# Kernel optimization log

Measured on AMD Instinct MI355X. Metric: run time of the kernel, lower is better.

Reference implementation:

```python
import jax, jax.numpy as jnp
import numpy as np

B, T, C, K, NH, HID, L, NC = 16, 500, 512, 7, 8, 2048, 3, 2
HD = C // NH
SCALE = float(1.0 / np.sqrt(HD))


def setup_inputs() -> dict:
    key = jax.random.key(0)
    ks = jax.random.split(key, 24)
    rn = lambda k, sh, s=0.02: jax.random.normal(k, sh, jnp.float32) * s
    return {
        'x': jax.random.normal(ks[0], (B, T, C), jnp.float32),
        'dw_w': rn(ks[1], (L, NC, C, 1, K)),   # depthwise conv kernels (groups=C)
        'dw_b': rn(ks[2], (L, NC, C)),
        'pw_w': rn(ks[3], (L, NC, C, C)),       # pointwise 1x1 conv weights [out,in]
        'pw_b': rn(ks[4], (L, NC, C)),
        'cln_g': jnp.ones((L, NC, C), jnp.float32),
        'cln_b': jnp.zeros((L, NC, C), jnp.float32),
        'wq': rn(ks[5], (L, C, C)), 'bq': rn(ks[6], (L, C)),
        'wk': rn(ks[7], (L, C, C)), 'bk': rn(ks[8], (L, C)),
        'wv': rn(ks[9], (L, C, C)), 'bv': rn(ks[10], (L, C)),
        'wo': rn(ks[11], (L, C, C)), 'bo': rn(ks[12], (L, C)),
        'aln_g': jnp.ones((L, C), jnp.float32), 'aln_b': jnp.zeros((L, C), jnp.float32),
        'w1': rn(ks[13], (L, HID, C)), 'b1': rn(ks[14], (L, HID)),
        'w2': rn(ks[15], (L, C, HID)), 'b2': rn(ks[16], (L, C)),
        'fln_g': jnp.ones((L, C), jnp.float32), 'fln_b': jnp.zeros((L, C), jnp.float32),
    }


def _ln(x, g, b):
    m = x.mean(-1, keepdims=True)
    v = ((x - m) ** 2).mean(-1, keepdims=True)
    return (x - m) / jnp.sqrt(v + 1e-5) * g + b


def _conv_block(x, w, b, pw, pb, g, be):
    # x: (B, C, T). Depthwise conv (groups=C), padding K//2 keeps T.
    out = jax.lax.conv_general_dilated(
        x, w, window_strides=(1,), padding=[(K // 2, K // 2)],
        feature_group_count=C, dimension_numbers=('NCH', 'OIH', 'NCH')) + b[None, :, None]
    out = jnp.einsum('bct,oc->bot', out, pw) + pb[None, :, None]  # pointwise 1x1
    out = _ln(out.transpose(0, 2, 1), g, be).transpose(0, 2, 1)
    return out


def _attn(x, wq, bq, wk, bk, wv, bv, wo, bo):
    Bx, Tx, Cx = x.shape
    def split(h):
        return h.reshape(Bx, Tx, NH, HD).transpose(0, 2, 1, 3)  # (B,H,T,HD)
    q = split(x @ wq.T + bq)
    k = split(x @ wk.T + bk)
    v = split(x @ wv.T + bv)
    att = jnp.einsum('bhqd,bhkd->bhqk', q, k) * SCALE
    mask = jnp.tril(jnp.ones((Tx, Tx), bool))
    att = jnp.where(mask, att, -1e10)
    att = jax.nn.softmax(att, axis=-1)
    y = jnp.einsum('bhqk,bhkd->bhqd', att, v)
    y = y.transpose(0, 2, 1, 3).reshape(Bx, Tx, Cx)
    return y @ wo.T + bo


def _block(x, l, dw_w, dw_b, pw_w, pw_b, cln_g, cln_b, wq, bq, wk, bk, wv, bv,
           wo, bo, aln_g, aln_b, w1, b1, w2, b2, fln_g, fln_b):
    out = x.transpose(0, 2, 1)  # (B, C, T)
    for c in range(NC):
        out = _conv_block(out, dw_w[l, c], dw_b[l, c], pw_w[l, c], pw_b[l, c],
                          cln_g[l, c], cln_b[l, c])
    out = out.transpose(0, 2, 1)  # (B, T, C)
    out = _attn(out, wq[l], bq[l], wk[l], bk[l], wv[l], bv[l], wo[l], bo[l])
    out = _ln(out, aln_g[l], aln_b[l])
    out = _ln(jax.nn.relu(out @ w1[l].T + b1[l]) @ w2[l].T + b2[l], fln_g[l], fln_b[l])
    return out  # eval mode: dropouts are identity


def reference(x, dw_w, dw_b, pw_w, pw_b, cln_g, cln_b, wq, bq, wk, bk, wv, bv,
              wo, bo, aln_g, aln_b, w1, b1, w2, b2, fln_g, fln_b):
    outs = []
    h = x
    for l in range(L):
        h = _block(h, l, dw_w, dw_b, pw_w, pw_b, cln_g, cln_b, wq, bq, wk, bk,
                   wv, bv, wo, bo, aln_g, aln_b, w1, b1, w2, b2, fln_g, fln_b)
        outs.append(h)
    return tuple(outs)
```

## Files before the change

### kernel.cpp

```cpp
#include <hip/hip_runtime.h>
#include <hip/hip_bf16.h>

namespace {
constexpr int B = 16, T = 500, C = 512, KW = 7, NH = 8, HD = 64, HID = 2048;
constexpr int M = B * T;
constexpr float SCALE = 0.125f;
constexpr int BTC = B * T * C;
constexpr int CC = C * C;
constexpr int SEG_PW0 = 0;
constexpr int SEG_PW1 = CC;
constexpr int SEG_WQ  = 2 * CC;
constexpr int SEG_WK  = 3 * CC;
constexpr int SEG_WV  = 4 * CC;
constexpr int SEG_WO  = 5 * CC;
constexpr int SEG_W1  = 6 * CC;
constexpr int SEG_W2  = 6 * CC + HID * C;
constexpr int SEG_END = 6 * CC + 2 * HID * C;
}

typedef short s16x8 __attribute__((ext_vector_type(8)));
typedef float f32x4v __attribute__((ext_vector_type(4)));
typedef unsigned short u16x4 __attribute__((ext_vector_type(4)));

__device__ __forceinline__ unsigned int bfrne(float f) {
  unsigned int u = __float_as_uint(f);
  return (u + 0x7fffu + ((u >> 16) & 1u)) >> 16;
}
__device__ __forceinline__ unsigned int pack2(float a, float b) {
  return bfrne(a) | (bfrne(b) << 16);
}

__global__ __launch_bounds__(256) void cvtw_kernel(
    const float* __restrict__ pw0, const float* __restrict__ pw1,
    const float* __restrict__ wqp, const float* __restrict__ wkp,
    const float* __restrict__ wvp, const float* __restrict__ wop,
    const float* __restrict__ w1p, const float* __restrict__ w2p,
    unsigned short* __restrict__ dst) {
  size_t e = ((size_t)blockIdx.x * 256 + threadIdx.x) * 8;
  const float* src;
  size_t off;
  if      (e < SEG_PW1) { src = pw0; off = e - SEG_PW0; }
  else if (e < SEG_WQ)  { src = pw1; off = e - SEG_PW1; }
  else if (e < SEG_WK)  { src = wqp; off = e - SEG_WQ; }
  else if (e < SEG_WV)  { src = wkp; off = e - SEG_WK; }
  else if (e < SEG_WO)  { src = wvp; off = e - SEG_WV; }
  else if (e < SEG_W1)  { src = wop; off = e - SEG_WO; }
  else if (e < SEG_W2)  { src = w1p; off = e - SEG_W1; }
  else                  { src = w2p; off = e - SEG_W2; }
  float4 a = *(const float4*)(src + off);
  float4 b = *(const float4*)(src + off + 4);
  uint4 o;
  o.x = pack2(a.x, a.y); o.y = pack2(a.z, a.w);
  o.z = pack2(b.x, b.y); o.w = pack2(b.z, b.w);
  *(uint4*)(dst + e) = o;
}

__global__ __launch_bounds__(256) void biascat_kernel(
    const float* __restrict__ bq, const float* __restrict__ bk,
    const float* __restrict__ bv, float* __restrict__ dst) {
  int i = blockIdx.x * 256 + threadIdx.x;
  float v = (i < 512) ? bq[i] : (i < 1024 ? bk[i - 512] : bv[i - 1024]);
  dst[i] = v;
}

template <bool XBF, bool RELU, bool YBF>
__global__ __launch_bounds__(256) void gemm_mfma(
    const void* __restrict__ Xv, const unsigned short* __restrict__ Wb,
    const float* __restrict__ bias, void* __restrict__ Yv, int N, int K) {
  __shared__ unsigned short As[2][128 * 40];
  __shared__ unsigned short Bs[2][128 * 40];
  const int tid = threadIdx.x;
  const int n0 = blockIdx.x * 128, m0 = blockIdx.y * 128;
  const int w = tid >> 6, lane = tid & 63;
  const int mh = (w & 1) * 64, nh = (w >> 1) * 64;
  const int quad = lane >> 4, r15 = lane & 15;

  const int row0 = tid >> 2,           kq0 = (tid & 3) * 8;
  const int row1 = (tid + 256) >> 2,   kq1 = (tid & 3) * 8;
  const int xr0 = min(m0 + row0, M - 1), xr1 = min(m0 + row1, M - 1);
  const int wr0 = n0 + row0, wr1 = n0 + row1;

  f32x4v acc[4][4];
#pragma unroll
  for (int i = 0; i < 4; ++i)
#pragma unroll
    for (int j = 0; j < 4; ++j) acc[i][j] = {0.f, 0.f, 0.f, 0.f};

  auto loadX = [&](int k0, int xr, int kq) -> uint4 {
    if (XBF) {
      return *(const uint4*)((const unsigned short*)Xv + (size_t)xr * K + k0 + kq);
    } else {
      const float* xp = (const float*)Xv + (size_t)xr * K + k0 + kq;
      float4 a = *(const float4*)xp;
      float4 b = *(const float4*)(xp + 4);
      uint4 o;
      o.x = pack2(a.x, a.y); o.y = pack2(a.z, a.w);
      o.z = pack2(b.x, b.y); o.w = pack2(b.z, b.w);
      return o;
    }
  };
  auto loadW = [&](int k0, int wr, int kq) -> uint4 {
    return *(const uint4*)(Wb + (size_t)wr * K + k0 + kq);
  };

  uint4 xv0 = loadX(0, xr0, kq0), xv1 = loadX(0, xr1, kq1);
  uint4 wv0 = loadW(0, wr0, kq0), wv1 = loadW(0, wr1, kq1);
  *(uint4*)&As[0][row0 * 40 + kq0] = xv0;
  *(uint4*)&As[0][row1 * 40 + kq1] = xv1;
  *(uint4*)&Bs[0][row0 * 40 + kq0] = wv0;
  *(uint4*)&Bs[0][row1 * 40 + kq1] = wv1;
  int cur = 0;
  const int nk = K / 32;
  for (int c = 0; c < nk; ++c) {
    __syncthreads();
    if (c + 1 < nk) {
      int k0 = (c + 1) * 32;
      xv0 = loadX(k0, xr0, kq0); xv1 = loadX(k0, xr1, kq1);
      wv0 = loadW(k0, wr0, kq0); wv1 = loadW(k0, wr1, kq1);
    }
    const unsigned short* Ac = As[cur];
    const unsigned short* Bc = Bs[cur];
    s16x8 af[4], bg[4];
#pragma unroll
    for (int im = 0; im < 4; ++im)
      af[im] = *(const s16x8*)&Ac[(mh + im * 16 + r15) * 40 + quad * 8];
#pragma unroll
    for (int in = 0; in < 4; ++in)
      bg[in] = *(const s16x8*)&Bc[(nh + in * 16 + r15) * 40 + quad * 8];
#pragma unroll
    for (int in = 0; in < 4; ++in)
#pragma unroll
      for (int im = 0; im < 4; ++im)
        acc[im][in] = __builtin_amdgcn_mfma_f32_16x16x32_bf16(
            af[im], bg[in], acc[im][in], 0, 0, 0);
    if (c + 1 < nk) {
      int nx = cur ^ 1;
      *(uint4*)&As[nx][row0 * 40 + kq0] = xv0;
      *(uint4*)&As[nx][row1 * 40 + kq1] = xv1;
      *(uint4*)&Bs[nx][row0 * 40 + kq0] = wv0;
      *(uint4*)&Bs[nx][row1 * 40 + kq1] = wv1;
      cur = nx;
    }
  }
#pragma unroll
  for (int in = 0; in < 4; ++in) {
    int col = n0 + nh + in * 16 + r15;
    float bv = bias[col];
#pragma unroll
    for (int im = 0; im < 4; ++im) {
      int rowb = m0 + mh + im * 16 + quad * 4;
#pragma unroll
      for (int r = 0; r < 4; ++r) {
        int row = rowb + r;
        if (row < M) {
          float v = acc[im][in][r] + bv;
          if (RELU) v = fmaxf(v, 0.f);
          if (YBF)
            ((unsigned short*)Yv)[(size_t)row * N + col] =
                (unsigned short)bfrne(v);
          else
            ((float*)Yv)[(size_t)row * N + col] = v;
        }
      }
    }
  }
}

__global__ __launch_bounds__(256) void dwconv_kernel(
    const float* __restrict__ X, const float* __restrict__ W,
    const float* __restrict__ bias, unsigned short* __restrict__ Y) {
  int gid = blockIdx.x * 256 + threadIdx.x;
  int b = blockIdx.y;
  int e = gid * 2;
  int t = e >> 9;
  int c = e & 511;
  float acc0 = bias[c], acc1 = bias[c + 1];
  size_t base = (size_t)b * T * C;
#pragma unroll
  for (int k = 0; k < KW; ++k) {
    int tt = t + k - 3;
    if (tt >= 0 && tt < T) {
      float2 xv = *(const float2*)&X[base + (size_t)tt * C + c];
      acc0 += xv.x * W[c * KW + k];
      acc1 += xv.y * W[(c + 1) * KW + k];
    }
  }
  *(unsigned int*)&Y[base + e] = pack2(acc0, acc1);
}

template <bool DUAL>
__global__ __launch_bounds__(256) void ln_kernel(
    const float* __restrict__ X, const float* __restrict__ g,
    const float* __restrict__ bta, float* __restrict__ Y,
    unsigned short* __restrict__ Yb) {
  int row = blockIdx.x * 4 + (threadIdx.x >> 6);
  int lane = threadIdx.x & 63;
  const float* x = X + (size_t)row * C + lane * 8;
  float4 a = *(const float4*)x;
  float4 b2 = *(const float4*)(x + 4);
  float v[8] = {a.x, a.y, a.z, a.w, b2.x, b2.y, b2.z, b2.w};
  float s = 0.f, ss = 0.f;
#pragma unroll
  for (int i = 0; i < 8; ++i) {
    s += v[i];
    ss += v[i] * v[i];
  }
#pragma unroll
  for (int off = 32; off; off >>= 1) {
    s += __shfl_xor(s, off);
    ss += __shfl_xor(ss, off);
  }
  float mean = s * (1.f / C);
  float var = ss * (1.f / C) - mean * mean;
  var = fmaxf(var, 0.f);
  float rstd = rsqrtf(var + 1e-5f);
  float4 g0 = *(const float4*)(g + lane * 8);
  float4 g1 = *(const float4*)(g + lane * 8 + 4);
  float4 be0 = *(const float4*)(bta + lane * 8);
  float4 be1 = *(const float4*)(bta + lane * 8 + 4);
  float gg[8] = {g0.x, g0.y, g0.z, g0.w, g1.x, g1.y, g1.z, g1.w};
  float bb[8] = {be0.x, be0.y, be0.z, be0.w, be1.x, be1.y, be1.z, be1.w};
  float o[8];
#pragma unroll
  for (int i = 0; i < 8; ++i) o[i] = (v[i] - mean) * rstd * gg[i] + bb[i];
  float* y = Y + (size_t)row * C + lane * 8;
  float4 w0 = {o[0], o[1], o[2], o[3]};
  float4 w1 = {o[4], o[5], o[6], o[7]};
  *(float4*)y = w0;
  *(float4*)(y + 4) = w1;
  if (DUAL) {
    uint4 ob;
    ob.x = pack2(o[0], o[1]); ob.y = pack2(o[2], o[3]);
    ob.z = pack2(o[4], o[5]); ob.w = pack2(o[6], o[7]);
    *(uint4*)(Yb + (size_t)row * C + lane * 8) = ob;
  }
}

__global__ __launch_bounds__(256) void attn_mfma_kernel(
    const unsigned short* __restrict__ QKV, unsigned short* __restrict__ Yb) {
  constexpr int QS = 3 * C;
  constexpr int LDK = 72;
  __shared__ __align__(16) unsigned short Ks[64 * LDK];
  __shared__ __align__(16) unsigned short Vt[64 * LDK];
  __shared__ __align__(16) unsigned short Ps[4][16 * LDK];
  const int tid = threadIdx.x;
  const int lane = tid & 63, w = tid >> 6;
  const int quad = lane >> 4, r15 = lane & 15;
  const int qt = blockIdx.x, hh = blockIdx.y, b = blockIdx.z;
  const int q0 = qt * 64;
  const size_t hbase = (size_t)hh * HD;

  s16x8 qa[2];
  {
    int qr = min(q0 + w * 16 + r15, T - 1);
    const unsigned short* qp = QKV + ((size_t)b * T + qr) * QS + hbase;
#pragma unroll
    for (int ks = 0; ks < 2; ++ks)
      qa[ks] = *(const s16x8*)(qp + ks * 32 + quad * 8);
  }

  f32x4v oacc[4];
  float mm[4], ll[4];
#pragma unroll
  for (int i = 0; i < 4; ++i) {
    oacc[i] = {0.f, 0.f, 0.f, 0.f};
    mm[i] = -1e30f;
    ll[i] = 0.f;
  }

  const int krow = tid >> 2, kd = (tid & 3) * 16;
  const int vk4 = (tid >> 4) * 4, vd4 = (tid & 15) * 4;

  const int kend = min(q0 + 63, T - 1);
  for (int key0 = 0; key0 <= kend; key0 += 64) {
    __syncthreads();
    {
      int key = key0 + krow;
      if (key < T) {
        const unsigned short* kp =
            QKV + ((size_t)b * T + key) * QS + C + hbase + kd;
        uint4 k0 = *(const uint4*)kp;
        uint4 k1 = *(const uint4*)(kp + 8);
        *(uint4*)&Ks[krow * LDK + kd] = k0;
        *(uint4*)&Ks[krow * LDK + kd + 8] = k1;
      } else {
        uint4 z = {0u, 0u, 0u, 0u};
        *(uint4*)&Ks[krow * LDK + kd] = z;
        *(uint4*)&Ks[krow * LDK + kd + 8] = z;
      }
    }
    {
      u16x4 va[4];
#pragma unroll
      for (int j = 0; j < 4; ++j) {
        int key = key0 + vk4 + j;
        if (key < T) {
          va[j] = *(const u16x4*)(QKV + ((size_t)b * T + key) * QS + 2 * C +
                                  hbase + vd4);
        } else {
          va[j] = (u16x4){0, 0, 0, 0};
        }
      }
#pragma unroll
      for (int i = 0; i < 4; ++i) {
        uint2 o2;
        o2.x = (unsigned int)va[0][i] | ((unsigned int)va[1][i] << 16);
        o2.y = (unsigned int)va[2][i] | ((unsigned int)va[3][i] << 16);
        *(uint2*)&Vt[(vd4 + i) * LDK + vk4] = o2;
      }
    }
    __syncthreads();

    f32x4v sa[4];
#pragma unroll
    for (int nt = 0; nt < 4; ++nt) {
      s16x8 kb0 = *(const s16x8*)&Ks[(nt * 16 + r15) * LDK + quad * 8];
      s16x8 kb1 = *(const s16x8*)&Ks[(nt * 16 + r15) * LDK + 32 + quad * 8];
      f32x4v z = {0.f, 0.f, 0.f, 0.f};
      z = __builtin_amdgcn_mfma_f32_16x16x32_bf16(qa[0], kb0, z, 0, 0, 0);
      z = __builtin_amdgcn_mfma_f32_16x16x32_bf16(qa[1], kb1, z, 0, 0, 0);
      sa[nt] = z;
    }
    const bool diag = (key0 == q0);

#pragma unroll
    for (int r = 0; r < 4; ++r) {
      int q = q0 + w * 16 + quad * 4 + r;
      float sv[4];
#pragma unroll
      for (int nt = 0; nt < 4; ++nt) {
        sv[nt] = sa[nt][r] * SCALE;
        if (diag && (key0 + nt * 16 + r15 > q)) sv[nt] = -1e30f;
      }
      float mx = fmaxf(fmaxf(sv[0], sv[1]), fmaxf(sv[2], sv[3]));
      mx = fmaxf(mx, __shfl_xor(mx, 8));
      mx = fmaxf(mx, __shfl_xor(mx, 4));
      mx = fmaxf(mx, __shfl_xor(mx, 2));
      mx = fmaxf(mx, __shfl_xor(mx, 1));
      float mnew = fmaxf(mm[r], mx);
      float alpha = __expf(mm[r] - mnew);
      float ps = 0.f;
#pragma unroll
      for (int nt = 0; nt < 4; ++nt) {
        float p = __expf(sv[nt] - mnew);
        ps += p;
        Ps[w][(quad * 4 + r) * LDK + nt * 16 + r15] =
            (unsigned short)bfrne(p);
      }
      ps += __shfl_xor(ps, 8);
      ps += __shfl_xor(ps, 4);
      ps += __shfl_xor(ps, 2);
      ps += __shfl_xor(ps, 1);
      ll[r] = ll[r] * alpha + ps;
      mm[r] = mnew;
#pragma unroll
      for (int dt = 0; dt < 4; ++dt) oacc[dt][r] *= alpha;
    }
    asm volatile("s_waitcnt lgkmcnt(0)" ::: "memory");
    __builtin_amdgcn_sched_barrier(0);

    s16x8 pa0 = *(const s16x8*)&Ps[w][r15 * LDK + quad * 8];
    s16x8 pa1 = *(const s16x8*)&Ps[w][r15 * LDK + 32 + quad * 8];
#pragma unroll
    for (int dt = 0; dt < 4; ++dt) {
      s16x8 vb0 = *(const s16x8*)&Vt[(dt * 16 + r15) * LDK + quad * 8];
      s16x8 vb1 = *(const s16x8*)&Vt[(dt * 16 + r15) * LDK + 32 + quad * 8];
      oacc[dt] =
          __builtin_amdgcn_mfma_f32_16x16x32_bf16(pa0, vb0, oacc[dt], 0, 0, 0);
      oacc[dt] =
          __builtin_amdgcn_mfma_f32_16x16x32_bf16(pa1, vb1, oacc[dt], 0, 0, 0);
    }
  }

#pragma unroll
  for (int r = 0; r < 4; ++r) {
    int q = q0 + w * 16 + quad * 4 + r;
    if (q < T) {
      float inv = 1.f / ll[r];
      unsigned short* yp = Yb + ((size_t)b * T + q) * C + hbase;
#pragma unroll
      for (int dt = 0; dt < 4; ++dt)
        yp[dt * 16 + r15] = (unsigned short)bfrne(oacc[dt][r] * inv);
    }
  }
}

extern "C" void kernel_launch(void* const* d_in, const int* in_sizes, int n_in,
                              void* d_out, int out_size, void* d_ws,
                              size_t ws_size, hipStream_t stream) {
  const float* x     = (const float*)d_in[0];
  const float* dw_w  = (const float*)d_in[1];
  const float* dw_b  = (const float*)d_in[2];
  const float* pw_w  = (const float*)d_in[3];
  const float* pw_b  = (const float*)d_in[4];
  const float* cln_g = (const float*)d_in[5];
  const float* cln_b = (const float*)d_in[6];
  const float* wq    = (const float*)d_in[7];
  const float* bq    = (const float*)d_in[8];
  const float* wk    = (const float*)d_in[9];
  const float* bk    = (const float*)d_in[10];
  const float* wv    = (const float*)d_in[11];
  const float* bv    = (const float*)d_in[12];
  const float* wo    = (const float*)d_in[13];
  const float* bo    = (const float*)d_in[14];
  const float* aln_g = (const float*)d_in[15];
  const float* aln_b = (const float*)d_in[16];
  const float* w1    = (const float*)d_in[17];
  const float* b1    = (const float*)d_in[18];
  const float* w2    = (const float*)d_in[19];
  const float* b2    = (const float*)d_in[20];
  const float* fln_g = (const float*)d_in[21];
  const float* fln_b = (const float*)d_in[22];

  float* ws = (float*)d_ws;
  float* A  = ws;
  float* Bf = ws + (size_t)BTC;
  float* R0 = ws + (size_t)2 * BTC;
  float* R1 = ws + (size_t)3 * BTC;
  float* R2 = ws + (size_t)4 * BTC;
  unsigned short* WA = (unsigned short*)(ws + (size_t)5 * BTC);
  float* out = (float*)d_out;

  unsigned short* xbf   = (unsigned short*)Bf;
  unsigned short* qkvbf = (unsigned short*)R0;
  unsigned short* fbf   = (unsigned short*)R2;
  unsigned short* hbf   = (unsigned short*)A;
  float* qkvb = A;

  dim3 blk(256);
  dim3 gemmC(C / 128, 63);
  dim3 gemmQKV(3 * C / 128, 63);
  dim3 gemmH(HID / 128, 63);
  dim3 convG(T * C / 512, B);
  dim3 attnG((T + 63) / 64, NH, B);
  int cvtwB = SEG_END / 2048;

  for (int l = 0; l < 3; ++l) {
    float* h = out + (size_t)l * BTC;
    const float* hin = (l == 0) ? x : out + (size_t)(l - 1) * BTC;
    cvtw_kernel<<<cvtwB, blk, 0, stream>>>(
        pw_w + (size_t)(2 * l) * CC, pw_w + (size_t)(2 * l + 1) * CC,
        wq + (size_t)l * CC, wk + (size_t)l * CC, wv + (size_t)l * CC,
        wo + (size_t)l * CC, w1 + (size_t)l * HID * C,
        w2 + (size_t)l * C * HID, WA);
    biascat_kernel<<<6, blk, 0, stream>>>(bq + (size_t)l * C,
                                          bk + (size_t)l * C,
                                          bv + (size_t)l * C, qkvb);
    for (int cb = 0; cb < 2; ++cb) {
      int lc = l * 2 + cb;
      const float* src = (cb == 0) ? hin : h;
      dwconv_kernel<<<convG, blk, 0, stream>>>(src, dw_w + (size_t)lc * C * KW,
                                               dw_b + (size_t)lc * C, xbf);
      gemm_mfma<true, false, false><<<gemmC, blk, 0, stream>>>(
          xbf, WA + (cb ? SEG_PW1 : SEG_PW0), pw_b + (size_t)lc * C, R0, C, C);
      if (cb == 0)
        ln_kernel<false><<<M / 4, blk, 0, stream>>>(
            R0, cln_g + (size_t)lc * C, cln_b + (size_t)lc * C, h, nullptr);
      else
        ln_kernel<true><<<M / 4, blk, 0, stream>>>(
            R0, cln_g + (size_t)lc * C, cln_b + (size_t)lc * C, h, xbf);
    }
    gemm_mfma<true, false, true><<<gemmQKV, blk, 0, stream>>>(
        xbf, WA + SEG_WQ, qkvb, qkvbf, 3 * C, C);
    attn_mfma_kernel<<<attnG, blk, 0, stream>>>(qkvbf, xbf);
    gemm_mfma<true, false, false><<<gemmC, blk, 0, stream>>>(
        xbf, WA + SEG_WO, bo + (size_t)l * C, R1, C, C);
    ln_kernel<true><<<M / 4, blk, 0, stream>>>(
        R1, aln_g + (size_t)l * C, aln_b + (size_t)l * C, h, fbf);
    gemm_mfma<true, true, true><<<gemmH, blk, 0, stream>>>(
        fbf, WA + SEG_W1, b1 + (size_t)l * HID, hbf, HID, C);
    gemm_mfma<true, false, false><<<gemmC, blk, 0, stream>>>(
        hbf, WA + SEG_W2, b2 + (size_t)l * C, R0, C, HID);
    ln_kernel<false><<<M / 4, blk, 0, stream>>>(
        R0, fln_g + (size_t)l * C, fln_b + (size_t)l * C, h, nullptr);
  }
}
```

Measured before the change: 1.067 ms.

## Use direct global-to-LDS loads with triple buffering and XCD-aware tile remap in GEMM

The bf16 GEMM now copies A and B tiles straight from global memory into LDS with global_load_lds, replacing the staging through registers. LDS becomes a three-deep ring with vmcnt-based waits, so two tiles are in flight while the current one is computed, and the padded layout is replaced by an XOR swizzle to avoid bank conflicts. Workgroup IDs are also remapped so that consecutive tiles land on the same XCD, which should improve L2 reuse. The risks are the hand-written swizzle and waitcnt logic, which must exactly match how the hardware scatters the async LDS writes, and the removal of the fp32-input path.

```diff
diff --git a/kernel.cpp b/kernel.cpp
--- a/kernel.cpp
+++ b/kernel.cpp
@@ -28,6 +28,13 @@
 }
 __device__ __forceinline__ unsigned int pack2(float a, float b) {
   return bfrne(a) | (bfrne(b) << 16);
+}
+
+__device__ __forceinline__ void gl_lds16(const unsigned short* g,
+                                         unsigned short* l) {
+  __builtin_amdgcn_global_load_lds(
+      (const __attribute__((address_space(1))) void*)g,
+      (__attribute__((address_space(3))) void*)l, 16, 0, 0);
 }
 
 __global__ __launch_bounds__(256) void cvtw_kernel(
@@ -63,22 +70,51 @@
   dst[i] = v;
 }
 
-template <bool XBF, bool RELU, bool YBF>
+template <bool RELU, bool YBF>
 __global__ __launch_bounds__(256) void gemm_mfma(
-    const void* __restrict__ Xv, const unsigned short* __restrict__ Wb,
-    const float* __restrict__ bias, void* __restrict__ Yv, int N, int K) {
-  __shared__ unsigned short As[2][128 * 40];
-  __shared__ unsigned short Bs[2][128 * 40];
+    const unsigned short* __restrict__ Xb,
+    const unsigned short* __restrict__ Wb, const float* __restrict__ bias,
+    void* __restrict__ Yv, int N, int K) {
+  __shared__ unsigned short As[3][128 * 32];
+  __shared__ unsigned short Bs[3][128 * 32];
   const int tid = threadIdx.x;
-  const int n0 = blockIdx.x * 128, m0 = blockIdx.y * 128;
   const int w = tid >> 6, lane = tid & 63;
+  const int quad = lane >> 4, r15 = lane & 15;
+
+  const int gx = gridDim.x;
+  const int nwg = gx * gridDim.y;
+  const int orig = blockIdx.y * gx + blockIdx.x;
+  const int q8 = nwg >> 3, r8 = nwg & 7;
+  const int xcd = orig & 7, sidx = orig >> 3;
+  const int tile =
+      (xcd < r8 ? xcd * (q8 + 1) : r8 * (q8 + 1) + (xcd - r8) * q8) + sidx;
+  const int n0 = (tile % gx) * 128;
+  const int m0 = (tile / gx) * 128;
+
+  const int pf = tid >> 2;
+  const int cch = tid & 3;
+  const int P = pf & 15;
+  const int Lr = ((P & 3) << 2) | (P >> 2);
+  const int lrow = (pf >> 4) * 16 + Lr;
+  const int gch = cch ^ (Lr & 3);
+  const size_t xa0 = (size_t)min(m0 + lrow, M - 1) * K + gch * 8;
+  const size_t xa1 = (size_t)min(m0 + lrow + 64, M - 1) * K + gch * 8;
+  const size_t wa0 = (size_t)(n0 + lrow) * K + gch * 8;
+  const size_t wa1 = (size_t)(n0 + lrow + 64) * K + gch * 8;
+  const int wbase = w * 512;
+
+  auto issue = [&](int buf, int k0) {
+    gl_lds16(Xb + xa0 + k0, &As[buf][wbase]);
+    gl_lds16(Xb + xa1 + k0, &As[buf][2048 + wbase]);
+    gl_lds16(Wb + wa0 + k0, &Bs[buf][wbase]);
+    gl_lds16(Wb + wa1 + k0, &Bs[buf][2048 + wbase]);
+  };
+
   const int mh = (w & 1) * 64, nh = (w >> 1) * 64;
-  const int quad = lane >> 4, r15 = lane & 15;
-
-  const int row0 = tid >> 2,           kq0 = (tid & 3) * 8;
-  const int row1 = (tid + 256) >> 2,   kq1 = (tid & 3) * 8;
-  const int xr0 = min(m0 + row0, M - 1), xr1 = min(m0 + row1, M - 1);
-  const int wr0 = n0 + row0, wr1 = n0 + row1;
+  const int bsw = ((r15 & 3) << 2) | (r15 >> 2);
+  const int chl = (quad ^ (r15 & 3)) * 8;
+  const int aoff = (mh + bsw) * 32 + chl;
+  const int boff = (nh + bsw) * 32 + chl;
 
   f32x4v acc[4][4];
 #pragma unroll
@@ -86,61 +122,35 @@
 #pragma unroll
     for (int j = 0; j < 4; ++j) acc[i][j] = {0.f, 0.f, 0.f, 0.f};
 
-  auto loadX = [&](int k0, int xr, int kq) -> uint4 {
-    if (XBF) {
-      return *(const uint4*)((const unsigned short*)Xv + (size_t)xr * K + k0 + kq);
-    } else {
-      const float* xp = (const float*)Xv + (size_t)xr * K + k0 + kq;
-      float4 a = *(const float4*)xp;
-      float4 b = *(const float4*)(xp + 4);
-      uint4 o;
-      o.x = pack2(a.x, a.y); o.y = pack2(a.z, a.w);
-      o.z = pack2(b.x, b.y); o.w = pack2(b.z, b.w);
-      return o;
-    }
-  };
-  auto loadW = [&](int k0, int wr, int kq) -> uint4 {
-    return *(const uint4*)(Wb + (size_t)wr * K + k0 + kq);
-  };
-
-  uint4 xv0 = loadX(0, xr0, kq0), xv1 = loadX(0, xr1, kq1);
-  uint4 wv0 = loadW(0, wr0, kq0), wv1 = loadW(0, wr1, kq1);
-  *(uint4*)&As[0][row0 * 40 + kq0] = xv0;
-  *(uint4*)&As[0][row1 * 40 + kq1] = xv1;
-  *(uint4*)&Bs[0][row0 * 40 + kq0] = wv0;
-  *(uint4*)&Bs[0][row1 * 40 + kq1] = wv1;
-  int cur = 0;
   const int nk = K / 32;
+  issue(0, 0);
+  issue(1, 32);
+  int cur = 0, nx2 = 2;
   for (int c = 0; c < nk; ++c) {
-    __syncthreads();
-    if (c + 1 < nk) {
-      int k0 = (c + 1) * 32;
-      xv0 = loadX(k0, xr0, kq0); xv1 = loadX(k0, xr1, kq1);
-      wv0 = loadW(k0, wr0, kq0); wv1 = loadW(k0, wr1, kq1);
-    }
+    if (c + 1 < nk)
+      asm volatile("s_waitcnt vmcnt(4)" ::: "memory");
+    else
+      asm volatile("s_waitcnt vmcnt(0)" ::: "memory");
+    __builtin_amdgcn_s_barrier();
+    asm volatile("" ::: "memory");
+    if (c + 2 < nk) issue(nx2, (c + 2) * 32);
     const unsigned short* Ac = As[cur];
     const unsigned short* Bc = Bs[cur];
     s16x8 af[4], bg[4];
 #pragma unroll
     for (int im = 0; im < 4; ++im)
-      af[im] = *(const s16x8*)&Ac[(mh + im * 16 + r15) * 40 + quad * 8];
+      af[im] = *(const s16x8*)&Ac[aoff + im * 512];
 #pragma unroll
     for (int in = 0; in < 4; ++in)
-      bg[in] = *(const s16x8*)&Bc[(nh + in * 16 + r15) * 40 + quad * 8];
+      bg[in] = *(const s16x8*)&Bc[boff + in * 512];
 #pragma unroll
     for (int in = 0; in < 4; ++in)
 #pragma unroll
       for (int im = 0; im < 4; ++im)
         acc[im][in] = __builtin_amdgcn_mfma_f32_16x16x32_bf16(
             af[im], bg[in], acc[im][in], 0, 0, 0);
-    if (c + 1 < nk) {
-      int nx = cur ^ 1;
-      *(uint4*)&As[nx][row0 * 40 + kq0] = xv0;
-      *(uint4*)&As[nx][row1 * 40 + kq1] = xv1;
-      *(uint4*)&Bs[nx][row0 * 40 + kq0] = wv0;
-      *(uint4*)&Bs[nx][row1 * 40 + kq1] = wv1;
-      cur = nx;
-    }
+    cur = (cur == 2) ? 0 : cur + 1;
+    nx2 = (nx2 == 2) ? 0 : nx2 + 1;
   }
 #pragma unroll
   for (int in = 0; in < 4; ++in) {
@@ -451,7 +461,7 @@
       const float* src = (cb == 0) ? hin : h;
       dwconv_kernel<<<convG, blk, 0, stream>>>(src, dw_w + (size_t)lc * C * KW,
                                                dw_b + (size_t)lc * C, xbf);
-      gemm_mfma<true, false, false><<<gemmC, blk, 0, stream>>>(
+      gemm_mfma<false, false><<<gemmC, blk, 0, stream>>>(
           xbf, WA + (cb ? SEG_PW1 : SEG_PW0), pw_b + (size_t)lc * C, R0, C, C);
       if (cb == 0)
         ln_kernel<false><<<M / 4, blk, 0, stream>>>(
@@ -460,16 +470,16 @@
         ln_kernel<true><<<M / 4, blk, 0, stream>>>(
             R0, cln_g + (size_t)lc * C, cln_b + (size_t)lc * C, h, xbf);
     }
-    gemm_mfma<true, false, true><<<gemmQKV, blk, 0, stream>>>(
+    gemm_mfma<false, true><<<gemmQKV, blk, 0, stream>>>(
         xbf, WA + SEG_WQ, qkvb, qkvbf, 3 * C, C);
     attn_mfma_kernel<<<attnG, blk, 0, stream>>>(qkvbf, xbf);
-    gemm_mfma<true, false, false><<<gemmC, blk, 0, stream>>>(
+    gemm_mfma<false, false><<<gemmC, blk, 0, stream>>>(
         xbf, WA + SEG_WO, bo + (size_t)l * C, R1, C, C);
     ln_kernel<true><<<M / 4, blk, 0, stream>>>(
         R1, aln_g + (size_t)l * C, aln_b + (size_t)l * C, h, fbf);
-    gemm_mfma<true, true, true><<<gemmH, blk, 0, stream>>>(
+    gemm_mfma<true, true><<<gemmH, blk, 0, stream>>>(
         fbf, WA + SEG_W1, b1 + (size_t)l * HID, hbf, HID, C);
-    gemm_mfma<true, false, false><<<gemmC, blk, 0, stream>>>(
+    gemm_mfma<false, false><<<gemmC, blk, 0, stream>>>(
         hbf, WA + SEG_W2, b2 + (size_t)l * C, R0, C, HID);
     ln_kernel<false><<<M / 4, blk, 0, stream>>>(
         R0, fln_g + (size_t)l * C, fln_b + (size_t)l * C, h, nullptr);
```

New measurement: 1.098 ms. +2.9%, slower.
